# Optimization experiments

Hardware: AMD Instinct MI355X
Metric: run time of the kernel (lower is better)

Reference implementation:

```python
import jax, jax.numpy as jnp
import numpy as np

B, Q, K, H, V = 32, 64, 512, 64, 64
NEG = -1e6


def setup_inputs() -> dict:
    key = jax.random.key(0)
    ks = jax.random.split(key, 7)
    queries = jax.random.normal(ks[0], (B, Q, H), dtype=jnp.float32)
    keys = jax.random.normal(ks[1], (B, K, H), dtype=jnp.float32)
    values = jax.random.normal(ks[2], (B, K, V), dtype=jnp.float32)
    valid_lens = jax.random.randint(ks[3], (B,), 1, K + 1, dtype=jnp.int32)
    # Linear weights stored as (in_features, out_features); x @ W == torch Linear
    Wq = jax.random.normal(ks[4], (H, H), dtype=jnp.float32) / np.sqrt(H)
    Wk = jax.random.normal(ks[5], (H, H), dtype=jnp.float32) / np.sqrt(H)
    wv = jax.random.normal(ks[6], (H,), dtype=jnp.float32) / np.sqrt(H)
    return {"queries": queries, "keys": keys, "values": values,
            "valid_lens": valid_lens, "Wq": Wq, "Wk": Wk, "wv": wv}


def reference(queries, keys, values, valid_lens, Wq, Wk, wv):
    q = jnp.einsum('bqd,dh->bqh', queries, Wq)          # (B,Q,H)
    k = jnp.einsum('bkd,dh->bkh', keys, Wk)             # (B,K,H)
    # additive (Bahdanau) features: (B,Q,K,H) broadcast intermediate
    feats = jnp.tanh(q[:, :, None, :] + k[:, None, :, :])
    scores = jnp.einsum('bqkh,h->bqk', feats, wv)       # (B,Q,K)
    # masked softmax over key axis: positions >= valid_len get -1e6
    mask = jnp.arange(K)[None, :] < valid_lens[:, None]  # (B,K)
    scores = jnp.where(mask[:, None, :], scores, NEG)
    attn = jax.nn.softmax(scores, axis=-1)              # (B,Q,K)
    return jnp.einsum('bqk,bkv->bqv', attn, values)     # (B,Q,V)
```

## Files before the change

kernel.cpp:

```cpp
#include <hip/hip_runtime.h>

#define NEG (-1e6f)

static constexpr int B = 32, Q = 64, K = 512, H = 64, V = 64;
static constexpr float C2LE = 2.8853900817779268f;
static constexpr float L2E  = 1.4426950408889634f;

typedef __attribute__((ext_vector_type(8))) short bf16x8;
typedef __attribute__((ext_vector_type(4))) float f32x4;

__device__ __forceinline__ float fexp2(float x) { return __builtin_amdgcn_exp2f(x); }
__device__ __forceinline__ float frcp(float x)  { return __builtin_amdgcn_rcpf(x); }

__device__ __forceinline__ short f2bf(float f) {
  union { float f; unsigned u; } v; v.f = f;
  unsigned r = v.u + 0x7fffu + ((v.u >> 16) & 1u);
  return (short)(r >> 16);
}

__global__ __launch_bounds__(256) void proj_kernel(
    const float* __restrict__ queries, const float* __restrict__ keys,
    const float* __restrict__ Wq, const float* __restrict__ Wk,
    const float* __restrict__ wv,
    float2* __restrict__ qAR, float* __restrict__ Ek)
{
  __shared__ float Wl[64 * 65];
  const int tid = threadIdx.x;
  const int lane = tid & 63;
  const int wave = __builtin_amdgcn_readfirstlane(tid >> 6);
  const int stripe0 = blockIdx.x * 4;
  const bool isQ = stripe0 < 128;
  const float* Wsrc = isQ ? Wq : Wk;

  #pragma unroll
  for (int i = 0; i < 16; ++i) {
    const int idx = tid + i * 256;
    Wl[(idx >> 6) * 65 + (idx & 63)] = Wsrc[idx];
  }
  __syncthreads();

  const int stripe = stripe0 + wave;
  const int row0 = stripe * 16;
  const int r = lane & 15, g = lane >> 4;
  const float* xbase = isQ ? (queries + (size_t)row0 * H)
                           : (keys + (size_t)(row0 - 2048) * H);

  bf16x8 afr[2];
  #pragma unroll
  for (int kb = 0; kb < 2; ++kb) {
    const float* px = xbase + (size_t)r * H + kb * 32 + g * 8;
    const float4 x0 = *(const float4*)px;
    const float4 x1 = *(const float4*)(px + 4);
    bf16x8 a;
    a[0]=f2bf(x0.x); a[1]=f2bf(x0.y); a[2]=f2bf(x0.z); a[3]=f2bf(x0.w);
    a[4]=f2bf(x1.x); a[5]=f2bf(x1.y); a[6]=f2bf(x1.z); a[7]=f2bf(x1.w);
    afr[kb] = a;
  }

  #pragma unroll
  for (int c = 0; c < 4; ++c) {
    const int col = c * 16 + r;
    f32x4 acc = {0.f, 0.f, 0.f, 0.f};
    #pragma unroll
    for (int kb = 0; kb < 2; ++kb) {
      bf16x8 bfr;
      #pragma unroll
      for (int j = 0; j < 8; ++j)
        bfr[j] = f2bf(Wl[(kb*32 + g*8 + j) * 65 + col]);
      acc = __builtin_amdgcn_mfma_f32_16x16x32_bf16(afr[kb], bfr, acc, 0, 0, 0);
    }
    const float wvv = wv[col];
    #pragma unroll
    for (int rr = 0; rr < 4; ++rr) {
      const int row = row0 + g * 4 + rr;
      const float s = fminf(15.f, fmaxf(-15.f, acc[rr])) * C2LE;
      if (isQ) {
        const float rq = fexp2(-s);
        qAR[(size_t)row * H + col] = make_float2(-2.f * wvv * rq, rq);
      } else {
        Ek[(size_t)(row - 2048) * H + col] = fexp2(s);
      }
    }
  }
}

__global__ __launch_bounds__(1024, 8) void attn_kernel(
    const float2* __restrict__ qAR, const float* __restrict__ Ek,
    const float* __restrict__ values, const int* __restrict__ vlens,
    float* __restrict__ out)
{
  __shared__ float pp[2][4][K];
  __shared__ float part[16][4][V];
  __shared__ float red[4][4][2];

  const int tid = threadIdx.x, lane = tid & 63;
  const int wave = __builtin_amdgcn_readfirstlane(tid >> 6);
  const int b = blockIdx.x >> 4, q0 = (blockIdx.x & 15) << 2;
  const int vlen = vlens[b];
  const float2* ar0 = qAR + ((size_t)b * Q + q0) * H;

  {
    const int key = tid & 511;
    const int half = __builtin_amdgcn_readfirstlane(tid >> 9);
    const float* ekrow = Ek + ((size_t)b * K + key) * H + half * 32;
    const float2* arh = ar0 + half * 32;
    float a0 = 0.f, a1 = 0.f, a2 = 0.f, a3 = 0.f;
    #pragma unroll
    for (int hc = 0; hc < 32; hc += 8) {
      float ek[8];
      *(float4*)(ek + 0) = *(const float4*)(ekrow + hc + 0);
      *(float4*)(ek + 4) = *(const float4*)(ekrow + hc + 4);
      #pragma unroll
      for (int j = 0; j < 8; ++j) {
        const float2 v0 = arh[0*H + hc + j];
        const float2 v1 = arh[1*H + hc + j];
        const float2 v2 = arh[2*H + hc + j];
        const float2 v3 = arh[3*H + hc + j];
        a0 = fmaf(v0.x, frcp(v0.y + ek[j]), a0);
        a1 = fmaf(v1.x, frcp(v1.y + ek[j]), a1);
        a2 = fmaf(v2.x, frcp(v2.y + ek[j]), a2);
        a3 = fmaf(v3.x, frcp(v3.y + ek[j]), a3);
      }
    }
    pp[half][0][key] = a0; pp[half][1][key] = a1;
    pp[half][2][key] = a2; pp[half][3][key] = a3;
  }
  __syncthreads();

  const int qi = wave & 3, quarter = wave >> 2;
  const int kq = quarter * 128 + lane * 2;
  float2 s;
  {
    const float2 u0 = *(const float2*)&pp[0][qi][kq];
    const float2 u1 = *(const float2*)&pp[1][qi][kq];
    s.x = (kq     < vlen) ? u0.x + u1.x : NEG;
    s.y = (kq + 1 < vlen) ? u0.y + u1.y : NEG;
    float m = fmaxf(s.x, s.y);
    #pragma unroll
    for (int off = 32; off; off >>= 1) m = fmaxf(m, __shfl_xor(m, off, 64));
    if (lane == 0) red[qi][quarter][0] = m;
  }
  __syncthreads();
  {
    const float m = fmaxf(fmaxf(red[qi][0][0], red[qi][1][0]),
                          fmaxf(red[qi][2][0], red[qi][3][0]));
    s.x = fexp2((s.x - m) * L2E);
    s.y = fexp2((s.y - m) * L2E);
    *(float2*)&pp[0][qi][kq] = s;
    float sum = s.x + s.y;
    #pragma unroll
    for (int off = 32; off; off >>= 1) sum += __shfl_xor(sum, off, 64);
    if (lane == 0) red[qi][quarter][1] = sum;
  }
  __syncthreads();

  {
    const int kb = wave * 32;
    const float* vb = values + ((size_t)b * K + kb) * V + lane;
    float a0 = 0.f, a1 = 0.f, a2 = 0.f, a3 = 0.f;
    #pragma unroll
    for (int k4 = 0; k4 < 32; k4 += 4) {
      const float4 p0 = *(const float4*)&pp[0][0][kb + k4];
      const float4 p1 = *(const float4*)&pp[0][1][kb + k4];
      const float4 p2 = *(const float4*)&pp[0][2][kb + k4];
      const float4 p3 = *(const float4*)&pp[0][3][kb + k4];
      const float v0 = vb[(size_t)(k4 + 0) * V];
      const float v1 = vb[(size_t)(k4 + 1) * V];
      const float v2 = vb[(size_t)(k4 + 2) * V];
      const float v3 = vb[(size_t)(k4 + 3) * V];
      a0 = fmaf(p0.x,v0, fmaf(p0.y,v1, fmaf(p0.z,v2, fmaf(p0.w,v3, a0))));
      a1 = fmaf(p1.x,v0, fmaf(p1.y,v1, fmaf(p1.z,v2, fmaf(p1.w,v3, a1))));
      a2 = fmaf(p2.x,v0, fmaf(p2.y,v1, fmaf(p2.z,v2, fmaf(p2.w,v3, a2))));
      a3 = fmaf(p3.x,v0, fmaf(p3.y,v1, fmaf(p3.z,v2, fmaf(p3.w,v3, a3))));
    }
    part[wave][0][lane] = a0; part[wave][1][lane] = a1;
    part[wave][2][lane] = a2; part[wave][3][lane] = a3;
  }
  __syncthreads();

  if (wave < 4) {
    const float inv = frcp(red[wave][0][1] + red[wave][1][1] +
                           red[wave][2][1] + red[wave][3][1]);
    float o = 0.f;
    #pragma unroll
    for (int w = 0; w < 16; ++w) o += part[w][wave][lane];
    out[((size_t)b * Q + q0 + wave) * V + lane] = o * inv;
  }
}

extern "C" void kernel_launch(void* const* d_in, const int* in_sizes, int n_in,
                              void* d_out, int out_size, void* d_ws, size_t ws_size,
                              hipStream_t stream) {
  const float* queries = (const float*)d_in[0];
  const float* keys    = (const float*)d_in[1];
  const float* values  = (const float*)d_in[2];
  const int*   vlens   = (const int*)d_in[3];
  const float* Wq      = (const float*)d_in[4];
  const float* Wk      = (const float*)d_in[5];
  const float* wv      = (const float*)d_in[6];
  float* out = (float*)d_out;

  float2* qAR = (float2*)d_ws;
  float*  Ek  = (float*)(qAR + (size_t)B*Q*H);

  proj_kernel<<<(B*Q + B*K) / 64, 256, 0, stream>>>(queries, keys, Wq, Wk, wv, qAR, Ek);
  attn_kernel<<<B*(Q/4), 1024, 0, stream>>>(qAR, Ek, values, vlens, out);
}
```

Measured before the change: 29.11 us.

## Transpose key features to h-major and broadcast query terms via readlane

The projection kernel now writes exp(2k) transposed as (B,H,K), using a swapped MFMA operand order so each lane holds one key. The attention kernel uses 512 threads, one key per thread over all 64 hidden dims, reading coalesced EkT columns. Per-query coefficients are held one per lane and broadcast with readlane instead of repeated global float2 loads. This removes the split-half partial-sum combine and halves the block size, at the cost of strided stores in proj and more serial work per thread.

```diff
diff --git a/kernel.cpp b/kernel.cpp
--- a/kernel.cpp
+++ b/kernel.cpp
@@ -18,11 +18,15 @@
   return (short)(r >> 16);
 }
 
+__device__ __forceinline__ float rdlane(float v, int l) {
+  return __uint_as_float(__builtin_amdgcn_readlane(__float_as_uint(v), l));
+}
+
 __global__ __launch_bounds__(256) void proj_kernel(
     const float* __restrict__ queries, const float* __restrict__ keys,
     const float* __restrict__ Wq, const float* __restrict__ Wk,
     const float* __restrict__ wv,
-    float2* __restrict__ qAR, float* __restrict__ Ek)
+    float2* __restrict__ qAR, float* __restrict__ EkT)
 {
   __shared__ float Wl[64 * 65];
   const int tid = threadIdx.x;
@@ -39,8 +43,7 @@
   }
   __syncthreads();
 
-  const int stripe = stripe0 + wave;
-  const int row0 = stripe * 16;
+  const int row0 = (stripe0 + wave) * 16;
   const int r = lane & 15, g = lane >> 4;
   const float* xbase = isQ ? (queries + (size_t)row0 * H)
                            : (keys + (size_t)(row0 - 2048) * H);
@@ -57,113 +60,124 @@
     afr[kb] = a;
   }
 
+  const int bb = isQ ? 0 : ((row0 - 2048) >> 9);
+  const int kbase = isQ ? 0 : ((row0 - 2048) & 511);
+
   #pragma unroll
-  for (int c = 0; c < 4; ++c) {
-    const int col = c * 16 + r;
+  for (int t = 0; t < 4; ++t) {
+    const int hcol = t * 16 + r;
     f32x4 acc = {0.f, 0.f, 0.f, 0.f};
     #pragma unroll
     for (int kb = 0; kb < 2; ++kb) {
-      bf16x8 bfr;
+      bf16x8 wfr;
       #pragma unroll
       for (int j = 0; j < 8; ++j)
-        bfr[j] = f2bf(Wl[(kb*32 + g*8 + j) * 65 + col]);
-      acc = __builtin_amdgcn_mfma_f32_16x16x32_bf16(afr[kb], bfr, acc, 0, 0, 0);
-    }
-    const float wvv = wv[col];
-    #pragma unroll
-    for (int rr = 0; rr < 4; ++rr) {
-      const int row = row0 + g * 4 + rr;
-      const float s = fminf(15.f, fmaxf(-15.f, acc[rr])) * C2LE;
-      if (isQ) {
+        wfr[j] = f2bf(Wl[(kb*32 + g*8 + j) * 65 + hcol]);
+      acc = isQ ? __builtin_amdgcn_mfma_f32_16x16x32_bf16(afr[kb], wfr, acc, 0, 0, 0)
+                : __builtin_amdgcn_mfma_f32_16x16x32_bf16(wfr, afr[kb], acc, 0, 0, 0);
+    }
+    if (isQ) {
+      const float wvv = wv[hcol];
+      #pragma unroll
+      for (int rr = 0; rr < 4; ++rr) {
+        const int row = row0 + g * 4 + rr;
+        const float s = fminf(15.f, fmaxf(-15.f, acc[rr])) * C2LE;
         const float rq = fexp2(-s);
-        qAR[(size_t)row * H + col] = make_float2(-2.f * wvv * rq, rq);
-      } else {
-        Ek[(size_t)(row - 2048) * H + col] = fexp2(s);
+        qAR[(size_t)row * H + hcol] = make_float2(-2.f * wvv * rq, rq);
       }
-    }
-  }
-}
-
-__global__ __launch_bounds__(1024, 8) void attn_kernel(
-    const float2* __restrict__ qAR, const float* __restrict__ Ek,
+    } else {
+      const int k = kbase + r;
+      #pragma unroll
+      for (int rr = 0; rr < 4; ++rr) {
+        const int h = t * 16 + g * 4 + rr;
+        const float s = fminf(15.f, fmaxf(-15.f, acc[rr])) * C2LE;
+        EkT[((size_t)bb * H + h) * K + k] = fexp2(s);
+      }
+    }
+  }
+}
+
+__global__ __launch_bounds__(512) void attn_kernel(
+    const float2* __restrict__ qAR, const float* __restrict__ EkT,
     const float* __restrict__ values, const int* __restrict__ vlens,
     float* __restrict__ out)
 {
-  __shared__ float pp[2][4][K];
-  __shared__ float part[16][4][V];
-  __shared__ float red[4][4][2];
+  __shared__ float p[4][K];
+  __shared__ float part[8][4][V];
+  __shared__ float red[4][2][2];
 
   const int tid = threadIdx.x, lane = tid & 63;
   const int wave = __builtin_amdgcn_readfirstlane(tid >> 6);
   const int b = blockIdx.x >> 4, q0 = (blockIdx.x & 15) << 2;
   const int vlen = vlens[b];
-  const float2* ar0 = qAR + ((size_t)b * Q + q0) * H;
-
-  {
-    const int key = tid & 511;
-    const int half = __builtin_amdgcn_readfirstlane(tid >> 9);
-    const float* ekrow = Ek + ((size_t)b * K + key) * H + half * 32;
-    const float2* arh = ar0 + half * 32;
+
+  float vA[4], vR[4];
+  {
+    const float2* ar0 = qAR + ((size_t)b * Q + q0) * H;
+    #pragma unroll
+    for (int qi = 0; qi < 4; ++qi) {
+      const float2 t = ar0[qi * H + lane];
+      vA[qi] = t.x; vR[qi] = t.y;
+    }
+  }
+
+  {
+    const float* ekp = EkT + (size_t)b * H * K + tid;
     float a0 = 0.f, a1 = 0.f, a2 = 0.f, a3 = 0.f;
     #pragma unroll
-    for (int hc = 0; hc < 32; hc += 8) {
+    for (int hc = 0; hc < 8; ++hc) {
       float ek[8];
-      *(float4*)(ek + 0) = *(const float4*)(ekrow + hc + 0);
-      *(float4*)(ek + 4) = *(const float4*)(ekrow + hc + 4);
+      #pragma unroll
+      for (int j = 0; j < 8; ++j) ek[j] = ekp[(size_t)(hc * 8 + j) * K];
       #pragma unroll
       for (int j = 0; j < 8; ++j) {
-        const float2 v0 = arh[0*H + hc + j];
-        const float2 v1 = arh[1*H + hc + j];
-        const float2 v2 = arh[2*H + hc + j];
-        const float2 v3 = arh[3*H + hc + j];
-        a0 = fmaf(v0.x, frcp(v0.y + ek[j]), a0);
-        a1 = fmaf(v1.x, frcp(v1.y + ek[j]), a1);
-        a2 = fmaf(v2.x, frcp(v2.y + ek[j]), a2);
-        a3 = fmaf(v3.x, frcp(v3.y + ek[j]), a3);
+        const int h = hc * 8 + j;
+        a0 = fmaf(rdlane(vA[0], h), frcp(rdlane(vR[0], h) + ek[j]), a0);
+        a1 = fmaf(rdlane(vA[1], h), frcp(rdlane(vR[1], h) + ek[j]), a1);
+        a2 = fmaf(rdlane(vA[2], h), frcp(rdlane(vR[2], h) + ek[j]), a2);
+        a3 = fmaf(rdlane(vA[3], h), frcp(rdlane(vR[3], h) + ek[j]), a3);
       }
     }
-    pp[half][0][key] = a0; pp[half][1][key] = a1;
-    pp[half][2][key] = a2; pp[half][3][key] = a3;
+    p[0][tid] = a0; p[1][tid] = a1; p[2][tid] = a2; p[3][tid] = a3;
   }
   __syncthreads();
 
-  const int qi = wave & 3, quarter = wave >> 2;
-  const int kq = quarter * 128 + lane * 2;
-  float2 s;
-  {
-    const float2 u0 = *(const float2*)&pp[0][qi][kq];
-    const float2 u1 = *(const float2*)&pp[1][qi][kq];
-    s.x = (kq     < vlen) ? u0.x + u1.x : NEG;
-    s.y = (kq + 1 < vlen) ? u0.y + u1.y : NEG;
-    float m = fmaxf(s.x, s.y);
+  const int qi = wave & 3, half = wave >> 2;
+  const int kb2 = half * 256 + lane * 4;
+  {
+    float s[4];
+    *(float4*)s = *(const float4*)&p[qi][kb2];
+    float m = NEG;
+    #pragma unroll
+    for (int j = 0; j < 4; ++j) {
+      s[j] = (kb2 + j < vlen) ? s[j] : NEG;
+      m = fmaxf(m, s[j]);
+    }
     #pragma unroll
     for (int off = 32; off; off >>= 1) m = fmaxf(m, __shfl_xor(m, off, 64));
-    if (lane == 0) red[qi][quarter][0] = m;
-  }
-  __syncthreads();
-  {
-    const float m = fmaxf(fmaxf(red[qi][0][0], red[qi][1][0]),
-                          fmaxf(red[qi][2][0], red[qi][3][0]));
-    s.x = fexp2((s.x - m) * L2E);
-    s.y = fexp2((s.y - m) * L2E);
-    *(float2*)&pp[0][qi][kq] = s;
-    float sum = s.x + s.y;
+    if (lane == 0) red[qi][half][0] = m;
+    __syncthreads();
+    m = fmaxf(red[qi][0][0], red[qi][1][0]);
+    float sum = 0.f;
+    #pragma unroll
+    for (int j = 0; j < 4; ++j) { s[j] = fexp2((s[j] - m) * L2E); sum += s[j]; }
+    *(float4*)&p[qi][kb2] = *(float4*)s;
     #pragma unroll
     for (int off = 32; off; off >>= 1) sum += __shfl_xor(sum, off, 64);
-    if (lane == 0) red[qi][quarter][1] = sum;
-  }
-  __syncthreads();
-
-  {
-    const int kb = wave * 32;
+    if (lane == 0) red[qi][half][1] = sum;
+    __syncthreads();
+  }
+
+  {
+    const int kb = wave * 64;
     const float* vb = values + ((size_t)b * K + kb) * V + lane;
     float a0 = 0.f, a1 = 0.f, a2 = 0.f, a3 = 0.f;
-    #pragma unroll
-    for (int k4 = 0; k4 < 32; k4 += 4) {
-      const float4 p0 = *(const float4*)&pp[0][0][kb + k4];
-      const float4 p1 = *(const float4*)&pp[0][1][kb + k4];
-      const float4 p2 = *(const float4*)&pp[0][2][kb + k4];
-      const float4 p3 = *(const float4*)&pp[0][3][kb + k4];
+    #pragma unroll 4
+    for (int k4 = 0; k4 < 64; k4 += 4) {
+      const float4 p0 = *(const float4*)&p[0][kb + k4];
+      const float4 p1 = *(const float4*)&p[1][kb + k4];
+      const float4 p2 = *(const float4*)&p[2][kb + k4];
+      const float4 p3 = *(const float4*)&p[3][kb + k4];
       const float v0 = vb[(size_t)(k4 + 0) * V];
       const float v1 = vb[(size_t)(k4 + 1) * V];
       const float v2 = vb[(size_t)(k4 + 2) * V];
@@ -179,11 +193,10 @@
   __syncthreads();
 
   if (wave < 4) {
-    const float inv = frcp(red[wave][0][1] + red[wave][1][1] +
-                           red[wave][2][1] + red[wave][3][1]);
+    const float inv = frcp(red[wave][0][1] + red[wave][1][1]);
     float o = 0.f;
     #pragma unroll
-    for (int w = 0; w < 16; ++w) o += part[w][wave][lane];
+    for (int w = 0; w < 8; ++w) o += part[w][wave][lane];
     out[((size_t)b * Q + q0 + wave) * V + lane] = o * inv;
   }
 }
@@ -201,8 +214,8 @@
   float* out = (float*)d_out;
 
   float2* qAR = (float2*)d_ws;
-  float*  Ek  = (float*)(qAR + (size_t)B*Q*H);
-
-  proj_kernel<<<(B*Q + B*K) / 64, 256, 0, stream>>>(queries, keys, Wq, Wk, wv, qAR, Ek);
-  attn_kernel<<<B*(Q/4), 1024, 0, stream>>>(qAR, Ek, values, vlens, out);
-}
+  float*  EkT = (float*)(qAR + (size_t)B*Q*H);
+
+  proj_kernel<<<(B*Q + B*K) / 64, 256, 0, stream>>>(queries, keys, Wq, Wk, wv, qAR, EkT);
+  attn_kernel<<<B*(Q/4), 512, 0, stream>>>(qAR, EkT, values, vlens, out);
+}
```

New measurement: 32.23 us. 1.11x slower.
